# Performance work log

Measured on AMD Instinct MI355X. Metric: run time of the kernel, lower is better.

Reference implementation:

```python
import jax, jax.numpy as jnp
import numpy as np
from jax import lax

M_RANGE = 1  # padding = m_range, kernel is (2*m_range+1)^2 = 9 classes of 3x3


def _conv(x, kernel):
    # torch F.conv2d (cross-correlation), stride 1, padding M_RANGE
    return lax.conv_general_dilated(
        x, kernel, window_strides=(1, 1),
        padding=[(M_RANGE, M_RANGE), (M_RANGE, M_RANGE)],
        dimension_numbers=('NCHW', 'OIHW', 'NCHW'))


def _construct_seg(ones, m_mask, m_kernel):
    # ones.expand_as(m_mask) * m_mask, then per-sample conv2d -> batched conv
    return _conv(ones * m_mask, m_kernel)  # [B,1,H,W]


def _construct_image(im, m_mask, appear, m_kernel):
    # im: [B,C,H,W]; m_mask: [B,K,H,W]; appear: [B,1,H,W]
    im = im * appear
    B, C, H, W = im.shape
    K = m_mask.shape[1]
    # fuse the python double loop: fold (B,C) into batch, conv K->1 once
    im_expand = (im[:, :, None, :, :] * m_mask[:, None, :, :, :]).reshape(B * C, K, H, W)
    return _conv(im_expand, m_kernel).reshape(B, C, H, W)


def setup_inputs() -> dict:
    key = jax.random.key(0)
    k0, k1, k2, k3 = jax.random.split(key, 4)
    B, C, H, W, K, N_INPUTS = 32, 3, 256, 256, 9, 2
    im_input_f = jax.random.uniform(k0, (B, N_INPUTS * C, H, W), dtype=jnp.float32)
    im_input_b = jax.random.uniform(k1, (B, N_INPUTS * C, H, W), dtype=jnp.float32)
    ones = jnp.ones((B, 1, H, W), dtype=jnp.float32)
    # gt motion masks: soft per-pixel distribution over K motion classes
    gt_motion_f = jax.nn.softmax(jax.random.normal(k2, (B, K, H, W), dtype=jnp.float32), axis=1)
    gt_motion_b = jax.nn.softmax(jax.random.normal(k3, (B, K, H, W), dtype=jnp.float32), axis=1)
    # one-hot displacement kernels: kernel i has a 1 at flat position i of the 3x3 window
    m_kernel = jnp.eye(K, dtype=jnp.float32).reshape(K, 3, 3)[None]  # [1,K,3,3]
    return {"im_input_f": im_input_f, "im_input_b": im_input_b, "ones": ones,
            "gt_motion_f": gt_motion_f, "gt_motion_b": gt_motion_b, "m_kernel": m_kernel}


def reference(im_input_f, im_input_b, ones, gt_motion_f, gt_motion_b, m_kernel):
    IM_CHANNEL = 3
    relu = jax.nn.relu
    m_mask_f, m_mask_b = gt_motion_f, gt_motion_b

    seg_f = _construct_seg(ones, m_mask_f, m_kernel)
    seg_b = _construct_seg(ones, m_mask_b, m_kernel)

    disappear_f = relu(seg_f - 1)
    appear_f = relu(1 - disappear_f)
    disappear_b = relu(seg_b - 1)
    appear_b = relu(1 - disappear_b)

    pred_f = _construct_image(im_input_f[:, -IM_CHANNEL:, :, :], m_mask_f, appear_f, m_kernel)
    pred_b = _construct_image(im_input_b[:, -IM_CHANNEL:, :, :], m_mask_b, appear_b, m_kernel)

    seg_f = 1 - relu(1 - seg_f)
    seg_b = 1 - relu(1 - seg_b)
    attn = (seg_f + 1e-5) / (seg_f + seg_b + 2e-5)  # [B,1,H,W], broadcasts over C
    pred = attn * pred_f + (1 - attn) * pred_b
    return (pred, m_mask_f, 1 - appear_f, attn, m_mask_b, 1 - appear_b, 1 - attn)
```

## Files before the change

### kernel.cpp

```cpp
#include <hip/hip_runtime.h>

#define BB 32
#define KK 9
#define CC 3
#define HH 256
#define WW 256
#define HW (HH * WW)

#define SZ_P ((size_t)BB * CC * HW)
#define SZ_M ((size_t)BB * KK * HW)
#define SZ_S ((size_t)BB * HW)

typedef float f4 __attribute__((ext_vector_type(4)));

__device__ __forceinline__ f4 ld4(const float* p) { return *(const f4*)p; }
__device__ __forceinline__ void ntst4(float* p, f4 v) {
  __builtin_nontemporal_store(v, (f4*)p);
}
__device__ __forceinline__ f4 vmax4(f4 a, f4 b) {
  return __builtin_elementwise_max(a, b);
}
__device__ __forceinline__ f4 app4(f4 s) {
  f4 one = {1.f, 1.f, 1.f, 1.f}, z = {0.f, 0.f, 0.f, 0.f};
  return vmax4(one - vmax4(s - one, z), z);
}
__device__ __forceinline__ float app1(float s) {
  return fmaxf(1.f - fmaxf(s - 1.f, 0.f), 0.f);
}
__device__ __forceinline__ f4 shiftwin(f4 v, int dx, int lane) {
  if (dx == 0) {
    float l = __shfl_up(v.w, 1);
    if (lane == 0) l = 0.f;
    return (f4){l, v.x, v.y, v.z};
  } else if (dx == 2) {
    float r = __shfl_down(v.x, 1);
    if (lane == 63) r = 0.f;
    return (f4){v.y, v.z, v.w, r};
  }
  return v;
}

__device__ __forceinline__ void run_pass(
    const float* __restrict__ g,
    const float* __restrict__ im,
    float* __restrict__ o_m,
    float (*s_seg)[WW],
    int w, int lane, int x0, int y0, int y, size_t hw,
    f4& seg_out, f4& p0, f4& p1, f4& p2) {
  const f4 z = {0.f, 0.f, 0.f, 0.f};
  f4 r[KK];
  f4 seg = z;
#pragma unroll
  for (int k = 0; k < KK; ++k) {
    const int dy = k / 3, dx = k % 3;
    int yr = y + dy - 1;
    f4 v = z;
    if ((unsigned)yr < HH)
      v = ld4(g + (size_t)k * HW + ((size_t)yr << 8) + x0);
    f4 wv = shiftwin(v, dx, lane);
    r[k] = wv;
    seg += wv;
    f4 c = (dy == 1) ? v : ld4(g + (size_t)k * HW + hw);
    ntst4(o_m + (size_t)k * HW + hw, c);
  }
  *(f4*)&s_seg[w + 1][x0] = seg;

  if (w < 2) {
    int lr = (w == 0) ? 0 : 9;
    int yh = (w == 0) ? y0 - 1 : y0 + 8;
    f4 s = z;
#pragma unroll
    for (int k = 0; k < KK; ++k) {
      const int dy = k / 3, dx = k % 3;
      int yr = yh + dy - 1;
      f4 v = z;
      if ((unsigned)yr < HH)
        v = ld4(g + (size_t)k * HW + ((size_t)yr << 8) + x0);
      s += shiftwin(v, dx, lane);
    }
    *(f4*)&s_seg[lr][x0] = s;
  }
  __syncthreads();

  p0 = z; p1 = z; p2 = z;
#pragma unroll
  for (int dy = 0; dy < 3; ++dy) {
    const float* srow = s_seg[w + dy];
    f4 sc = *(const f4*)&srow[x0];
    float sl = srow[(x0 == 0) ? 0 : (x0 - 1)];
    float sr = srow[(x0 == WW - 4) ? (WW - 1) : (x0 + 4)];
    f4 ac = app4(sc);
    float al = app1(sl), ar = app1(sr);

    int yr = y + dy - 1;
    f4 i0 = z, i1 = z, i2 = z;
    if ((unsigned)yr < HH) {
      size_t rb = ((size_t)yr << 8) + x0;
      i0 = ld4(im + rb);
      i1 = ld4(im + HW + rb);
      i2 = ld4(im + 2 * HW + rb);
    }
    float i0l = __shfl_up(i0.w, 1), i0r = __shfl_down(i0.x, 1);
    float i1l = __shfl_up(i1.w, 1), i1r = __shfl_down(i1.x, 1);
    float i2l = __shfl_up(i2.w, 1), i2r = __shfl_down(i2.x, 1);
#pragma unroll
    for (int dx = 0; dx < 3; ++dx) {
      const int k = 3 * dy + dx;
      f4 aw = (dx == 0) ? (f4){al, ac.x, ac.y, ac.z}
            : (dx == 2) ? (f4){ac.y, ac.z, ac.w, ar} : ac;
      f4 c = aw * r[k];
      f4 w0 = (dx == 0) ? (f4){i0l, i0.x, i0.y, i0.z}
            : (dx == 2) ? (f4){i0.y, i0.z, i0.w, i0r} : i0;
      f4 w1 = (dx == 0) ? (f4){i1l, i1.x, i1.y, i1.z}
            : (dx == 2) ? (f4){i1.y, i1.z, i1.w, i1r} : i1;
      f4 w2 = (dx == 0) ? (f4){i2l, i2.x, i2.y, i2.z}
            : (dx == 2) ? (f4){i2.y, i2.z, i2.w, i2r} : i2;
      p0 += c * w0;
      p1 += c * w1;
      p2 += c * w2;
    }
  }
  __syncthreads();
  seg_out = seg;
}

__global__ __launch_bounds__(512) void fused_binet_kernel(
    const float* __restrict__ im_f, const float* __restrict__ im_b,
    const float* __restrict__ gt_f, const float* __restrict__ gt_b,
    float* __restrict__ out) {
  __shared__ float s_seg[10][WW];

  int bid = blockIdx.x;
  int actual = ((bid & 7) << 7) | (bid >> 3);
  int b  = actual >> 5;
  int y0 = (actual & 31) << 3;

  int tid  = threadIdx.x;
  int w    = tid >> 6;
  int lane = tid & 63;
  int x0   = lane << 2;
  int y    = y0 + w;
  size_t hw = ((size_t)y << 8) + x0;

  const float* gf  = gt_f + (size_t)b * KK * HW;
  const float* gb  = gt_b + (size_t)b * KK * HW;
  const float* imf = im_f + ((size_t)b * 6 + 3) * HW;
  const float* imb = im_b + ((size_t)b * 6 + 3) * HW;

  float* o_mf     = out + SZ_P + (size_t)b * KK * HW;
  float* o_disf   = out + SZ_P + SZ_M;
  float* o_attn   = o_disf + SZ_S;
  float* o_mb     = o_attn + SZ_S + (size_t)b * KK * HW;
  float* o_disb   = o_attn + SZ_S + SZ_M;
  float* o_1mattn = o_disb + SZ_S;

  f4 segf, segb, pf0, pf1, pf2, pb0, pb1, pb2;
  run_pass(gf, imf, o_mf, s_seg, w, lane, x0, y0, y, hw, segf, pf0, pf1, pf2);
  run_pass(gb, imb, o_mb, s_seg, w, lane, x0, y0, y, hw, segb, pb0, pb1, pb2);

  f4 one = {1.f, 1.f, 1.f, 1.f}, z = {0.f, 0.f, 0.f, 0.f};
  f4 appf = app4(segf);
  f4 appb = app4(segb);
  f4 sfc = one - vmax4(one - segf, z);
  f4 sbc = one - vmax4(one - segb, z);
  f4 attn = (sfc + 1e-5f) / (sfc + sbc + 2e-5f);
  f4 at2 = one - attn;

  size_t sidx = (size_t)b * HW + hw;
  ntst4(o_disf + sidx, one - appf);
  ntst4(o_attn + sidx, attn);
  ntst4(o_disb + sidx, one - appb);
  ntst4(o_1mattn + sidx, one - attn);

  size_t pbase = (size_t)b * CC * HW + hw;
  ntst4(out + pbase,          attn * pf0 + at2 * pb0);
  ntst4(out + pbase + HW,     attn * pf1 + at2 * pb1);
  ntst4(out + pbase + 2 * HW, attn * pf2 + at2 * pb2);
}

extern "C" void kernel_launch(void* const* d_in, const int* in_sizes, int n_in,
                              void* d_out, int out_size, void* d_ws, size_t ws_size,
                              hipStream_t stream) {
  const float* im_f = (const float*)d_in[0];
  const float* im_b = (const float*)d_in[1];
  const float* gt_f = (const float*)d_in[3];
  const float* gt_b = (const float*)d_in[4];
  float* out = (float*)d_out;

  dim3 block(512);
  dim3 grid(BB * 32);

  fused_binet_kernel<<<grid, block, 0, stream>>>(im_f, im_b, gt_f, gt_b, out);
}
```

Baseline: 391.0 us.

## Shrink blocks to four rows, drop register-cached windows, double-buffer seg smem

The block shrinks from 8 rows with 512 threads to 4 rows with 256 threads, and the launch bound now requests 6 blocks per CU. The 9-register window cache is gone: the predict pass reloads the motion masks from global, which should cut register pressure and raise occupancy. Seg rows for both directions go into separate shared buffers, so there is one fewer barrier. Neighbour appear values now come from shuffles instead of scalar LDS reads. In exchange, halo rows are recomputed more often and the masks are loaded again, adding L2/global traffic.

```diff
diff --git a/kernel.cpp b/kernel.cpp
--- a/kernel.cpp
+++ b/kernel.cpp
@@ -24,9 +24,6 @@
   f4 one = {1.f, 1.f, 1.f, 1.f}, z = {0.f, 0.f, 0.f, 0.f};
   return vmax4(one - vmax4(s - one, z), z);
 }
-__device__ __forceinline__ float app1(float s) {
-  return fmaxf(1.f - fmaxf(s - 1.f, 0.f), 0.f);
-}
 __device__ __forceinline__ f4 shiftwin(f4 v, int dx, int lane) {
   if (dx == 0) {
     float l = __shfl_up(v.w, 1);
@@ -39,16 +36,15 @@
   }
   return v;
 }
+__device__ __forceinline__ f4 win(f4 v, float l, float r, int dx) {
+  if (dx == 0) return (f4){l, v.x, v.y, v.z};
+  if (dx == 2) return (f4){v.y, v.z, v.w, r};
+  return v;
+}
 
-__device__ __forceinline__ void run_pass(
-    const float* __restrict__ g,
-    const float* __restrict__ im,
-    float* __restrict__ o_m,
-    float (*s_seg)[WW],
-    int w, int lane, int x0, int y0, int y, size_t hw,
-    f4& seg_out, f4& p0, f4& p1, f4& p2) {
+__device__ __forceinline__ f4 seg_row(const float* __restrict__ g, int y,
+                                      int x0, int lane) {
   const f4 z = {0.f, 0.f, 0.f, 0.f};
-  f4 r[KK];
   f4 seg = z;
 #pragma unroll
   for (int k = 0; k < KK; ++k) {
@@ -57,45 +53,29 @@
     f4 v = z;
     if ((unsigned)yr < HH)
       v = ld4(g + (size_t)k * HW + ((size_t)yr << 8) + x0);
-    f4 wv = shiftwin(v, dx, lane);
-    r[k] = wv;
-    seg += wv;
-    f4 c = (dy == 1) ? v : ld4(g + (size_t)k * HW + hw);
-    ntst4(o_m + (size_t)k * HW + hw, c);
+    seg += shiftwin(v, dx, lane);
   }
-  *(f4*)&s_seg[w + 1][x0] = seg;
+  return seg;
+}
 
-  if (w < 2) {
-    int lr = (w == 0) ? 0 : 9;
-    int yh = (w == 0) ? y0 - 1 : y0 + 8;
-    f4 s = z;
-#pragma unroll
-    for (int k = 0; k < KK; ++k) {
-      const int dy = k / 3, dx = k % 3;
-      int yr = yh + dy - 1;
-      f4 v = z;
-      if ((unsigned)yr < HH)
-        v = ld4(g + (size_t)k * HW + ((size_t)yr << 8) + x0);
-      s += shiftwin(v, dx, lane);
-    }
-    *(f4*)&s_seg[lr][x0] = s;
-  }
-  __syncthreads();
-
+__device__ __forceinline__ void pred_pass(
+    const float* __restrict__ g, const float* __restrict__ im,
+    const float (*sseg)[WW], int w, int lane, int x0, int y,
+    f4& p0, f4& p1, f4& p2) {
+  const f4 z = {0.f, 0.f, 0.f, 0.f};
   p0 = z; p1 = z; p2 = z;
 #pragma unroll
   for (int dy = 0; dy < 3; ++dy) {
-    const float* srow = s_seg[w + dy];
-    f4 sc = *(const f4*)&srow[x0];
-    float sl = srow[(x0 == 0) ? 0 : (x0 - 1)];
-    float sr = srow[(x0 == WW - 4) ? (WW - 1) : (x0 + 4)];
+    int yr = y + dy - 1;
+    bool ok = (unsigned)yr < HH;
+    size_t rb = ((size_t)yr << 8) + x0;
+
+    f4 sc = *(const f4*)&sseg[w + dy][x0];
     f4 ac = app4(sc);
-    float al = app1(sl), ar = app1(sr);
+    float al = __shfl_up(ac.w, 1), ar = __shfl_down(ac.x, 1);
 
-    int yr = y + dy - 1;
     f4 i0 = z, i1 = z, i2 = z;
-    if ((unsigned)yr < HH) {
-      size_t rb = ((size_t)yr << 8) + x0;
+    if (ok) {
       i0 = ld4(im + rb);
       i1 = ld4(im + HW + rb);
       i2 = ld4(im + 2 * HW + rb);
@@ -103,37 +83,31 @@
     float i0l = __shfl_up(i0.w, 1), i0r = __shfl_down(i0.x, 1);
     float i1l = __shfl_up(i1.w, 1), i1r = __shfl_down(i1.x, 1);
     float i2l = __shfl_up(i2.w, 1), i2r = __shfl_down(i2.x, 1);
+
 #pragma unroll
     for (int dx = 0; dx < 3; ++dx) {
       const int k = 3 * dy + dx;
-      f4 aw = (dx == 0) ? (f4){al, ac.x, ac.y, ac.z}
-            : (dx == 2) ? (f4){ac.y, ac.z, ac.w, ar} : ac;
-      f4 c = aw * r[k];
-      f4 w0 = (dx == 0) ? (f4){i0l, i0.x, i0.y, i0.z}
-            : (dx == 2) ? (f4){i0.y, i0.z, i0.w, i0r} : i0;
-      f4 w1 = (dx == 0) ? (f4){i1l, i1.x, i1.y, i1.z}
-            : (dx == 2) ? (f4){i1.y, i1.z, i1.w, i1r} : i1;
-      f4 w2 = (dx == 0) ? (f4){i2l, i2.x, i2.y, i2.z}
-            : (dx == 2) ? (f4){i2.y, i2.z, i2.w, i2r} : i2;
-      p0 += c * w0;
-      p1 += c * w1;
-      p2 += c * w2;
+      f4 gv = z;
+      if (ok)
+        gv = ld4(g + (size_t)k * HW + rb);
+      f4 c = win(ac, al, ar, dx) * shiftwin(gv, dx, lane);
+      p0 += c * win(i0, i0l, i0r, dx);
+      p1 += c * win(i1, i1l, i1r, dx);
+      p2 += c * win(i2, i2l, i2r, dx);
     }
   }
-  __syncthreads();
-  seg_out = seg;
 }
 
-__global__ __launch_bounds__(512) void fused_binet_kernel(
+__global__ __launch_bounds__(256, 6) void fused_binet_kernel(
     const float* __restrict__ im_f, const float* __restrict__ im_b,
     const float* __restrict__ gt_f, const float* __restrict__ gt_b,
     float* __restrict__ out) {
-  __shared__ float s_seg[10][WW];
+  __shared__ float s_seg[2][6][WW];
 
   int bid = blockIdx.x;
-  int actual = ((bid & 7) << 7) | (bid >> 3);
-  int b  = actual >> 5;
-  int y0 = (actual & 31) << 3;
+  int actual = ((bid & 7) << 8) | (bid >> 3);
+  int b  = actual >> 6;
+  int y0 = (actual & 63) << 2;
 
   int tid  = threadIdx.x;
   int w    = tid >> 6;
@@ -154,9 +128,40 @@
   float* o_disb   = o_attn + SZ_S + SZ_M;
   float* o_1mattn = o_disb + SZ_S;
 
-  f4 segf, segb, pf0, pf1, pf2, pb0, pb1, pb2;
-  run_pass(gf, imf, o_mf, s_seg, w, lane, x0, y0, y, hw, segf, pf0, pf1, pf2);
-  run_pass(gb, imb, o_mb, s_seg, w, lane, x0, y0, y, hw, segb, pb0, pb1, pb2);
+  f4 segf = seg_row(gf, y, x0, lane);
+  *(f4*)&s_seg[0][w + 1][x0] = segf;
+  if (w == 0) {
+    f4 s = seg_row(gf, y0 - 1, x0, lane);
+    *(f4*)&s_seg[0][0][x0] = s;
+  } else if (w == 1) {
+    f4 s = seg_row(gf, y0 + 4, x0, lane);
+    *(f4*)&s_seg[0][5][x0] = s;
+  }
+  __syncthreads();
+
+  f4 segb = seg_row(gb, y, x0, lane);
+  *(f4*)&s_seg[1][w + 1][x0] = segb;
+  if (w == 0) {
+    f4 s = seg_row(gb, y0 - 1, x0, lane);
+    *(f4*)&s_seg[1][0][x0] = s;
+  } else if (w == 1) {
+    f4 s = seg_row(gb, y0 + 4, x0, lane);
+    *(f4*)&s_seg[1][5][x0] = s;
+  }
+
+#pragma unroll
+  for (int k = 0; k < KK; ++k)
+    ntst4(o_mf + (size_t)k * HW + hw, ld4(gf + (size_t)k * HW + hw));
+
+  f4 pf0, pf1, pf2;
+  pred_pass(gf, imf, s_seg[0], w, lane, x0, y, pf0, pf1, pf2);
+  __syncthreads();
+
+#pragma unroll
+  for (int k = 0; k < KK; ++k)
+    ntst4(o_mb + (size_t)k * HW + hw, ld4(gb + (size_t)k * HW + hw));
+  f4 pb0, pb1, pb2;
+  pred_pass(gb, imb, s_seg[1], w, lane, x0, y, pb0, pb1, pb2);
 
   f4 one = {1.f, 1.f, 1.f, 1.f}, z = {0.f, 0.f, 0.f, 0.f};
   f4 appf = app4(segf);
@@ -187,8 +192,8 @@
   const float* gt_b = (const float*)d_in[4];
   float* out = (float*)d_out;
 
-  dim3 block(512);
-  dim3 grid(BB * 32);
+  dim3 block(256);
+  dim3 grid(BB * 64);
 
   fused_binet_kernel<<<grid, block, 0, stream>>>(im_f, im_b, gt_f, gt_b, out);
 }
```

Result: slower. 618.5 us (+58.2%).
